# Kernel tuning notes

Hardware: AMD Instinct MI355X
Metric: run time of the kernel (lower is better)

## Reference

```python
import jax, jax.numpy as jnp
import numpy as np

C = 64      # n_feats
DG = 8      # deformable groups
K = 3       # kernel size


def _lrelu(v):
    return jnp.where(v >= 0, v, 0.1 * v)


def _conv3x3(v, w, b):
    out = jax.lax.conv_general_dilated(
        v, w, window_strides=(1, 1), padding=((1, 1), (1, 1)),
        dimension_numbers=('NCHW', 'OIHW', 'NCHW'))
    return out + b[None, :, None, None]


def _up2(v):
    # bilinear upsample x2, align_corners=True (separable gather + lerp)
    B, Cc, H, W = v.shape
    def coords(n):
        c = jnp.arange(2 * n, dtype=jnp.float32) * ((n - 1) / (2 * n - 1))
        i0 = jnp.floor(c).astype(jnp.int32)
        i1 = jnp.minimum(i0 + 1, n - 1)
        f = (c - i0).astype(v.dtype)
        return i0, i1, f
    y0, y1, fy = coords(H)
    x0, x1, fx = coords(W)
    t = v[:, :, y0, :] * (1 - fy)[None, None, :, None] + v[:, :, y1, :] * fy[None, None, :, None]
    return t[:, :, :, x0] * (1 - fx)[None, None, None, :] + t[:, :, :, x1] * fx[None, None, None, :]


def _deform_conv(x, offset, mask, w, b):
    # modulated deformable conv (DCNv2), stride=1, pad=1, dil=1
    B, Cc, H, W = x.shape
    K2 = K * K
    cpg = Cc // DG
    off_y = offset[:, :DG * K2].reshape(B, DG, K2, H, W)
    off_x = offset[:, DG * K2:].reshape(B, DG, K2, H, W)
    m = mask.reshape(B, DG, 1, K2, H, W)
    ky, kx = jnp.meshgrid(jnp.arange(K) - 1, jnp.arange(K) - 1, indexing='ij')
    ky = ky.reshape(K2).astype(x.dtype)
    kx = kx.reshape(K2).astype(x.dtype)
    # absolute sampling positions [B, DG, K2, H, W]
    py = off_y + ky[None, None, :, None, None] + jnp.arange(H, dtype=x.dtype)[None, None, None, :, None]
    px = off_x + kx[None, None, :, None, None] + jnp.arange(W, dtype=x.dtype)[None, None, None, None, :]
    y0f = jnp.floor(py)
    x0f = jnp.floor(px)
    wy = py - y0f
    wx = px - x0f
    y0 = y0f.astype(jnp.int32)
    x0 = x0f.astype(jnp.int32)
    xg = x.reshape(B, DG, cpg, H * W)
    def corner(yi, xi, wgt):
        valid = ((yi >= 0) & (yi < H) & (xi >= 0) & (xi < W)).astype(x.dtype)
        yc = jnp.clip(yi, 0, H - 1)
        xc = jnp.clip(xi, 0, W - 1)
        idx = (yc * W + xc).reshape(B, DG, 1, K2 * H * W)
        g = jnp.take_along_axis(xg, jnp.broadcast_to(idx, (B, DG, cpg, K2 * H * W)), axis=3)
        g = g.reshape(B, DG, cpg, K2, H, W)
        return g * (wgt * valid)[:, :, None]
    val = (corner(y0, x0, (1 - wy) * (1 - wx))
           + corner(y0, x0 + 1, (1 - wy) * wx)
           + corner(y0 + 1, x0, wy * (1 - wx))
           + corner(y0 + 1, x0 + 1, wy * wx))
    val = val * m
    wr = w.reshape(Cc, DG, cpg, K2)
    return jnp.einsum('bgckhw,ogck->bohw', val, wr) + b[None, :, None, None]


def setup_inputs() -> dict:
    key = jax.random.key(0)
    ks = jax.random.split(key, 18)
    B, H, W = 2, 128, 128
    def p(k, shape):
        return jax.random.normal(k, shape, jnp.float32) * 0.05
    return {
        'x': jax.random.normal(ks[0], (B, C, H, W), jnp.float32),
        'y': jax.random.normal(ks[1], (B, C, H, W), jnp.float32),
        'prev_offset': jax.random.normal(ks[2], (B, C, H // 2, W // 2), jnp.float32),
        'prev_stage_fea': jax.random.normal(ks[3], (B, C, H // 2, W // 2), jnp.float32),
        'w1': p(ks[4], (C, 2 * C, 3, 3)), 'b1': jnp.zeros((C,), jnp.float32),
        'w2': p(ks[5], (C, 2 * C, 3, 3)), 'b2': jnp.zeros((C,), jnp.float32),
        'w3': p(ks[6], (C, C, 3, 3)), 'b3': jnp.zeros((C,), jnp.float32),
        'w_off': p(ks[7], (DG * 3 * K * K, C, 3, 3)), 'b_off': jnp.zeros((DG * 3 * K * K,), jnp.float32),
        'w_dcn': p(ks[8], (C, C, 3, 3)), 'b_dcn': jnp.zeros((C,), jnp.float32),
        'w_fea': p(ks[9], (C, 2 * C, 3, 3)), 'b_fea': jnp.zeros((C,), jnp.float32),
    }


def reference(x, y, prev_offset, prev_stage_fea,
              w1, b1, w2, b2, w3, b3, w_off, b_off, w_dcn, b_dcn, w_fea, b_fea):
    prev_offset = _up2(prev_offset)
    off = _lrelu(_conv3x3(jnp.concatenate([x, y], axis=1), w1, b1))
    off = _lrelu(_conv3x3(jnp.concatenate([off, prev_offset * 2], axis=1), w2, b2))
    off = _lrelu(_conv3x3(off, w3, b3))
    # DCNv2Pack: offsets/mask predicted from the offset feature
    co = _conv3x3(off, w_off, b_off)
    o1, o2, m = jnp.split(co, 3, axis=1)
    dcn_offset = jnp.concatenate([o1, o2], axis=1)
    m = jax.nn.sigmoid(m)
    fea = _deform_conv(x, dcn_offset, m, w_dcn, b_dcn)
    prev_fea = _up2(prev_stage_fea)
    out = _lrelu(_conv3x3(jnp.concatenate([fea, prev_fea], axis=1), w_fea, b_fea))
    return (off, out)
```

## Files before the change

### kernel.cpp

```cpp
#include <hip/hip_runtime.h>
#include <math.h>

typedef __bf16 bf16x8 __attribute__((ext_vector_type(8)));
typedef float f32x4 __attribute__((ext_vector_type(4)));
typedef unsigned short u16;
typedef __attribute__((address_space(3))) unsigned int lds_u32;
typedef const __attribute__((address_space(1))) unsigned int glb_u32;

__device__ __forceinline__ u16 f2bf(float f) {
    unsigned int u = __builtin_bit_cast(unsigned int, f);
    unsigned int r = (u + 0x7FFFu + ((u >> 16) & 1u)) >> 16;
    return (u16)r;
}
__device__ __forceinline__ float bf2f(u16 u) {
    unsigned int v = ((unsigned int)u) << 16;
    return __builtin_bit_cast(float, v);
}
__device__ __forceinline__ unsigned int pack2(float a, float b) {
    return (unsigned int)f2bf(a) | ((unsigned int)f2bf(b) << 16);
}
__device__ __forceinline__ bf16x8 ld8(const u16* p) {
    uint4 u = *reinterpret_cast<const uint4*>(p);
    return __builtin_bit_cast(bf16x8, u);
}
__device__ __forceinline__ void gload_lds16(const u16* g, u16* l) {
#if __has_builtin(__builtin_amdgcn_global_load_lds)
    __builtin_amdgcn_global_load_lds((glb_u32*)g, (lds_u32*)l, 16, 0, 0);
#else
    *reinterpret_cast<uint4*>(l) = *reinterpret_cast<const uint4*>(g);
#endif
}

__device__ __forceinline__ void dev_zero(u16* base, int nimg, int C, int B, int tid) {
    int idx = B * 256 + tid;
    int c8 = C >> 3;
    int tot = nimg * 516 * c8;
    if (idx >= tot) return;
    int cb = idx % c8;
    int t = idx / c8;
    int pb = t % 516;
    int img = t / 516;
    int y, x;
    if (pb < 130)      { y = 0;        x = pb; }
    else if (pb < 260) { y = 129;      x = pb - 130; }
    else if (pb < 388) { y = pb - 259; x = 0; }
    else               { y = pb - 387; x = 129; }
    u16* d = base + ((size_t)img * 16900 + (size_t)y * 130 + x) * C + cb * 8;
    uint4 z = {0u, 0u, 0u, 0u};
    *reinterpret_cast<uint4*>(d) = z;
}

__device__ __forceinline__ void dev_repack(const float* w, u16* dst,
                                           int Cout, int Cin, int mode, int B, int tid) {
    int idx = B * 256 + tid;
    int total = Cout * Cin * 9;
    if (idx >= total) return;
    int kk = idx % 9;
    int t = idx / 9;
    int ci = t % Cin;
    int o = t / Cin;
    u16 v = f2bf(w[idx]);
    size_t d;
    if (mode == 0) d = (size_t)o * (9 * Cin) + kk * Cin + ci;
    else           d = (size_t)o * 576 + (ci >> 3) * 72 + kk * 8 + (ci & 7);
    dst[d] = v;
}

__device__ __forceinline__ void dev_to_nhwc8(const float* src, u16* dst,
                                             int c0, int Ctot, int B, int tid) {
    int b = B >> 7;
    int rem = B & 127;
    int q = rem >> 4;
    int p0 = ((rem & 15) * 256 + tid) * 4;
    int y = p0 >> 7, x = p0 & 127;
    const float* s = src + ((size_t)b * 64 + q * 8) * 16384 + p0;
    u16* dbase = dst + (((size_t)b * 16900) + (size_t)(y + 1) * 130 + (x + 1)) * Ctot
                 + c0 + q * 8;
    float4 f[8];
#pragma unroll
    for (int c = 0; c < 8; ++c)
        f[c] = *reinterpret_cast<const float4*>(s + (size_t)c * 16384);
    const float* fp = (const float*)f;
#pragma unroll
    for (int j = 0; j < 4; ++j) {
        uint4 u;
        u.x = pack2(fp[0 * 4 + j], fp[1 * 4 + j]);
        u.y = pack2(fp[2 * 4 + j], fp[3 * 4 + j]);
        u.z = pack2(fp[4 * 4 + j], fp[5 * 4 + j]);
        u.w = pack2(fp[6 * 4 + j], fp[7 * 4 + j]);
        *reinterpret_cast<uint4*>(dbase + (size_t)j * Ctot) = u;
    }
}

__device__ __forceinline__ void dev_up2_8(const float* src, u16* dst,
                                          int c0, int Ctot, float scale, int B, int tid) {
    int b = B >> 9;
    int rem = B & 511;
    int q = rem >> 6;
    int pix = (rem & 63) * 256 + tid;
    int y = pix >> 7, x = pix & 127;
    const float f = 63.0f / 127.0f;
    float cy = y * f, cx = x * f;
    float y0f = floorf(cy), x0f = floorf(cx);
    int y0 = (int)y0f, x0 = (int)x0f;
    int y1 = min(y0 + 1, 63), x1 = min(x0 + 1, 63);
    float fy = cy - y0f, fx = cx - x0f;
    float w00 = (1.f - fy) * (1.f - fx) * scale, w01 = (1.f - fy) * fx * scale;
    float w10 = fy * (1.f - fx) * scale, w11 = fy * fx * scale;
    int i00 = y0 * 64 + x0, i01 = y0 * 64 + x1, i10 = y1 * 64 + x0, i11 = y1 * 64 + x1;
    const float* s = src + ((size_t)b * 64 + q * 8) * 4096;
    float v[8];
#pragma unroll
    for (int c = 0; c < 8; ++c) {
        const float* p = s + (size_t)c * 4096;
        v[c] = w00 * p[i00] + w01 * p[i01] + w10 * p[i10] + w11 * p[i11];
    }
    uint4 u;
    u.x = pack2(v[0], v[1]); u.y = pack2(v[2], v[3]);
    u.z = pack2(v[4], v[5]); u.w = pack2(v[6], v[7]);
    u16* d = dst + (((size_t)b * 16900) + (size_t)(y + 1) * 130 + (x + 1)) * Ctot
             + c0 + q * 8;
    *reinterpret_cast<uint4*>(d) = u;
}

__global__ __launch_bounds__(256) void preproc(
    const float* __restrict__ x, const float* __restrict__ y,
    const float* __restrict__ prev_off, const float* __restrict__ prev_fea,
    const float* __restrict__ w1, const float* __restrict__ w2,
    const float* __restrict__ w3, const float* __restrict__ w_off,
    const float* __restrict__ w_dcn, const float* __restrict__ w_fea,
    u16* __restrict__ T1, u16* __restrict__ T3, u16* __restrict__ T9,
    u16* __restrict__ T4,
    u16* __restrict__ wq1, u16* __restrict__ wq2, u16* __restrict__ wq3,
    u16* __restrict__ wqo, u16* __restrict__ wqd, u16* __restrict__ wqf) {
    int B = blockIdx.x, tid = threadIdx.x;
    if (B < 1024) { dev_up2_8(prev_off, T3, 64, 128, 2.0f, B, tid); return; } B -= 1024;
    if (B < 1024) { dev_up2_8(prev_fea, T9, 64, 128, 1.0f, B, tid); return; } B -= 1024;
    if (B < 256) { dev_to_nhwc8(x, T1, 0, 128, B, tid); return; }       B -= 256;
    if (B < 256) { dev_to_nhwc8(y, T1, 64, 128, B, tid); return; }      B -= 256;
    if (B < 129) { dev_zero(T1, 4, 128, B, tid); return; }  B -= 129;
    if (B < 65)  { dev_zero(T9, 2, 128, B, tid); return; }  B -= 65;
    if (B < 65)  { dev_zero(T4, 4, 64, B, tid); return; }   B -= 65;
    if (B < 288) { dev_repack(w1, wq1, 64, 128, 0, B, tid); return; }   B -= 288;
    if (B < 288) { dev_repack(w2, wq2, 64, 128, 0, B, tid); return; }   B -= 288;
    if (B < 144) { dev_repack(w3, wq3, 64, 64, 0, B, tid); return; }    B -= 144;
    if (B < 486) { dev_repack(w_off, wqo, 216, 64, 0, B, tid); return; } B -= 486;
    if (B < 144) { dev_repack(w_dcn, wqd, 64, 64, 1, B, tid); return; } B -= 144;
    dev_repack(w_fea, wqf, 64, 128, 0, B, tid);
}

template<int CIN, int WAVES, int KSPLIT, int ACTM, bool NHWC_OUT, bool OUT_PAD, int NCHW_MODE>
__global__ __launch_bounds__(WAVES * 64) void conv_tile(
    const u16* __restrict__ in, const u16* __restrict__ wgt,
    const float* __restrict__ bias,
    u16* __restrict__ outN, int c0, int Ctot,
    void* __restrict__ outC, int Cout) {
    constexpr int T = WAVES * 64;
    constexpr int PXW = WAVES / KSPLIT;
    constexpr int BPR = 4 / PXW;
    constexpr int KCH = CIN / KSPLIT;
    constexpr int CSTEPS = KCH / 32;
    constexpr int MSK = (CIN == 128) ? 15 : 7;
    constexpr int RSH = (CIN == 128) ? 8 : 7;
    __shared__ __align__(16) u16 As[2][64 * CIN];

    const int tid = threadIdx.x;
    const int lane = tid & 63;
    const int wv = tid >> 6;
    const int kslice = wv % KSPLIT;
    const int pxc = wv / KSPLIT;
    const int gx = blockIdx.x;
    const int xh = gx % BPR;
    const int y = (gx / BPR) & 127;
    const int b = gx / (BPR * 128);
    const int mblk = blockIdx.y << 6;
    const int n0 = lane & 15;
    const int kq = lane >> 4;
    const int xbase = xh * (PXW * 32) + pxc * 32;

    const u16* inB = in + (size_t)b * 16900 * CIN;

#define STAGE(ss, bf) {                                                        \
        _Pragma("unroll")                                                      \
        for (int i_ = 0; i_ < (8 * CIN) / T; ++i_) {                           \
            int L_ = (i_ * T + tid) * 16;                                      \
            int row_ = L_ >> RSH;                                              \
            int c16_ = (L_ >> 4) & MSK;                                        \
            int sc_ = c16_ ^ (row_ & MSK);                                     \
            const u16* src_ = wgt + (size_t)(mblk + row_) * (9 * CIN)          \
                              + (ss) * CIN + sc_ * 8;                          \
            gload_lds16(src_, &As[bf][L_ >> 1]);                               \
        }                                                                      \
    }

    f32x4 acc[4][2] = {};

    STAGE(0, 0)
    __syncthreads();

    for (int s = 0; s < 9; ++s) {
        const int buf = s & 1;
        if (s < 8) STAGE(s + 1, buf ^ 1)

        const int dy = s / 3, dx = s - dy * 3;
        const u16* brow = inB + ((size_t)(y + dy) * 130 + (xbase + n0 + dx)) * CIN
                          + kq * 8;
        const u16* ab = &As[buf][0];
#pragma unroll
        for (int c = 0; c < CSTEPS; ++c) {
            const int kch = kslice * KCH + c * 32;
            bf16x8 b0 = ld8(brow + kch);
            bf16x8 b1 = ld8(brow + 16 * CIN + kch);
            const int colb = (((kch >> 3) + kq) ^ (n0 & MSK)) * 8;
            bf16x8 a0 = ld8(ab + (0 * 16 + n0) * CIN + colb);
            bf16x8 a1 = ld8(ab + (1 * 16 + n0) * CIN + colb);
            bf16x8 a2 = ld8(ab + (2 * 16 + n0) * CIN + colb);
            bf16x8 a3 = ld8(ab + (3 * 16 + n0) * CIN + colb);
            acc[0][0] = __builtin_amdgcn_mfma_f32_16x16x32_bf16(a0, b0, acc[0][0], 0, 0, 0);
            acc[0][1] = __builtin_amdgcn_mfma_f32_16x16x32_bf16(a0, b1, acc[0][1], 0, 0, 0);
            acc[1][0] = __builtin_amdgcn_mfma_f32_16x16x32_bf16(a1, b0, acc[1][0], 0, 0, 0);
            acc[1][1] = __builtin_amdgcn_mfma_f32_16x16x32_bf16(a1, b1, acc[1][1], 0, 0, 0);
            acc[2][0] = __builtin_amdgcn_mfma_f32_16x16x32_bf16(a2, b0, acc[2][0], 0, 0, 0);
            acc[2][1] = __builtin_amdgcn_mfma_f32_16x16x32_bf16(a2, b1, acc[2][1], 0, 0, 0);
            acc[3][0] = __builtin_amdgcn_mfma_f32_16x16x32_bf16(a3, b0, acc[3][0], 0, 0, 0);
            acc[3][1] = __builtin_amdgcn_mfma_f32_16x16x32_bf16(a3, b1, acc[3][1], 0, 0, 0);
        }
        __syncthreads();
    }
#undef STAGE

    if (KSPLIT == 2) {
        float* red = (float*)(&As[0][0]);
        if (kslice == 1) {
#pragma unroll
            for (int mt = 0; mt < 4; ++mt)
#pragma unroll
                for (int nt = 0; nt < 2; ++nt)
                    *reinterpret_cast<f32x4*>(
                        &red[((pxc * 8) + mt * 2 + nt) * 256 + lane * 4]) = acc[mt][nt];
        }
        __syncthreads();
        if (kslice == 1) return;
#pragma unroll
        for (int mt = 0; mt < 4; ++mt)
#pragma unroll
            for (int nt = 0; nt < 2; ++nt)
                acc[mt][nt] += *reinterpret_cast<const f32x4*>(
                    &red[((pxc * 8) + mt * 2 + nt) * 256 + lane * 4]);
    }

#pragma unroll
    for (int mt = 0; mt < 4; ++mt) {
        const int mbase = mblk + mt * 16 + kq * 4;
        float bs0 = 0.f, bs1 = 0.f, bs2 = 0.f, bs3 = 0.f;
        if (mbase < Cout) {
            bs0 = bias[mbase]; bs1 = bias[mbase + 1];
            bs2 = bias[mbase + 2]; bs3 = bias[mbase + 3];
        }
#pragma unroll
        for (int nt = 0; nt < 2; ++nt) {
            const int xx = xbase + nt * 16 + n0;
            float v0 = acc[mt][nt][0] + bs0, v1 = acc[mt][nt][1] + bs1;
            float v2 = acc[mt][nt][2] + bs2, v3 = acc[mt][nt][3] + bs3;
            if (ACTM == 1) {
                v0 = (v0 >= 0.f) ? v0 : 0.1f * v0;
                v1 = (v1 >= 0.f) ? v1 : 0.1f * v1;
                v2 = (v2 >= 0.f) ? v2 : 0.1f * v2;
                v3 = (v3 >= 0.f) ? v3 : 0.1f * v3;
            } else if (ACTM == 2) {
                if (mbase >= 144) {
                    v0 = 1.f / (1.f + expf(-v0));
                    v1 = 1.f / (1.f + expf(-v1));
                    v2 = 1.f / (1.f + expf(-v2));
                    v3 = 1.f / (1.f + expf(-v3));
                }
            }
            if (NHWC_OUT && mbase < Cout) {
                size_t pix = OUT_PAD ? ((size_t)(y + 1) * 130 + xx + 1)
                                     : ((size_t)y * 128 + xx);
                size_t off = ((size_t)b * (OUT_PAD ? 16900 : 16384) + pix) * Ctot + c0 + mbase;
                uint2 u;
                u.x = pack2(v0, v1); u.y = pack2(v2, v3);
                *reinterpret_cast<uint2*>(outN + off) = u;
            }
            if (NCHW_MODE == 1 && mbase < Cout) {
                float* oc = (float*)outC;
                size_t o = ((size_t)(b * Cout + mbase)) * 16384 + (size_t)y * 128 + xx;
                oc[o] = v0; oc[o + 16384] = v1;
                oc[o + 2 * 16384] = v2; oc[o + 3 * 16384] = v3;
            }
            if (NCHW_MODE == 2 && mbase < Cout) {
                u16* oc = (u16*)outC;
                size_t o = ((size_t)(b * Cout + mbase)) * 16384 + (size_t)y * 128 + xx;
                oc[o] = f2bf(v0); oc[o + 16384] = f2bf(v1);
                oc[o + 2 * 16384] = f2bf(v2); oc[o + 3 * 16384] = f2bf(v3);
            }
        }
    }
}

__global__ __launch_bounds__(256, 2) void dcn_fused(
    const u16* __restrict__ xn, const u16* __restrict__ co,
    const u16* __restrict__ wgt, const float* __restrict__ bias,
    u16* __restrict__ outN) {
    __shared__ u16 lw[64 * 584];
    {
        int t = threadIdx.x;
        int o = t >> 2, chunk = t & 3;
        const u16* src = wgt + o * 576 + chunk * 144;
        u16* dst = lw + o * 584 + chunk * 144;
#pragma unroll
        for (int i = 0; i < 18; ++i)
            *reinterpret_cast<uint4*>(dst + i * 8) =
                *reinterpret_cast<const uint4*>(src + i * 8);
    }
    __syncthreads();

    const int lane = threadIdx.x & 63;
    const int wv = threadIdx.x >> 6;
    const int half = blockIdx.x & 1;
    const int y = (blockIdx.x >> 1) & 127;
    const int b = blockIdx.x >> 8;
    const int n0 = lane & 15;
    const int kq = lane >> 4;
    const int xx = half * 64 + wv * 16 + n0;
    const int p = y * 128 + xx;

    const u16* cob = co + (size_t)b * 216 * 16384 + p;
    const u16* xb = xn + (size_t)b * 16900 * 128;

    float offy[18], offx[18], mvv[18];
#pragma unroll
    for (int cs = 0; cs < 18; ++cs) {
        int gk8 = cs * 4 + kq;
        offy[cs] = bf2f(cob[(size_t)gk8 * 16384]);
        offx[cs] = bf2f(cob[(size_t)(72 + gk8) * 16384]);
        mvv[cs]  = bf2f(cob[(size_t)(144 + gk8) * 16384]);
    }

    f32x4 acc[4] = {};
    float w00[2], w01[2], w10[2], w11[2];
    uint4 q00[2], q01[2], q10[2], q11[2];

#define DCN_GL(cs, st) {                                                       \
        int gk8_ = (cs) * 4 + kq;                                              \
        int g_ = (gk8_ * 57) >> 9;                                             \
        int kk_ = gk8_ - 9 * g_;                                               \
        int ky_ = (kk_ * 11) >> 5;                                             \
        int kx_ = kk_ - 3 * ky_;                                               \
        float py_ = offy[cs] + (float)(ky_ - 1) + (float)y;                    \
        float px_ = offx[cs] + (float)(kx_ - 1) + (float)xx;                   \
        float y0f_ = floorf(py_), x0f_ = floorf(px_);                          \
        float wy_ = py_ - y0f_, wx_ = px_ - x0f_;                              \
        int y0_ = (int)y0f_, x0_ = (int)x0f_, y1_ = y0_ + 1, x1_ = x0_ + 1;    \
        float m00_ = ((unsigned)y0_ < 128u && (unsigned)x0_ < 128u) ? 1.f : 0.f; \
        float m01_ = ((unsigned)y0_ < 128u && (unsigned)x1_ < 128u) ? 1.f : 0.f; \
        float m10_ = ((unsigned)y1_ < 128u && (unsigned)x0_ < 128u) ? 1.f : 0.f; \
        float m11_ = ((unsigned)y1_ < 128u && (unsigned)x1_ < 128u) ? 1.f : 0.f; \
        float mv_ = mvv[cs];                                                   \
        w00[st] = (1.f - wy_) * (1.f - wx_) * m00_ * mv_;                      \
        w01[st] = (1.f - wy_) * wx_ * m01_ * mv_;                              \
        w10[st] = wy_ * (1.f - wx_) * m10_ * mv_;                              \
        w11[st] = wy_ * wx_ * m11_ * mv_;                                      \
        int y0c_ = min(max(y0_, 0), 127), y1c_ = min(max(y1_, 0), 127);        \
        int x0c_ = min(max(x0_, 0), 127), x1c_ = min(max(x1_, 0), 127);        \
        const u16* xg_ = xb + g_ * 8;                                          \
        q00[st] = *reinterpret_cast<const uint4*>(xg_ + ((size_t)(y0c_ + 1) * 130 + x0c_ + 1) * 128); \
        q01[st] = *reinterpret_cast<const uint4*>(xg_ + ((size_t)(y0c_ + 1) * 130 + x1c_ + 1) * 128); \
        q10[st] = *reinterpret_cast<const uint4*>(xg_ + ((size_t)(y1c_ + 1) * 130 + x0c_ + 1) * 128); \
        q11[st] = *reinterpret_cast<const uint4*>(xg_ + ((size_t)(y1c_ + 1) * 130 + x1c_ + 1) * 128); \
    }

#define DCN_GU(cs, st) {                                                       \
        const unsigned int* a00_ = &q00[st].x; const unsigned int* a01_ = &q01[st].x; \
        const unsigned int* a10_ = &q10[st].x; const unsigned int* a11_ = &q11[st].x; \
        float r_[8];                                                           \
        _Pragma("unroll")                                                      \
        for (int c = 0; c < 8; ++c) {                                          \
            unsigned int u00_ = a00_[c >> 1], u01_ = a01_[c >> 1];             \
            unsigned int u10_ = a10_[c >> 1], u11_ = a11_[c >> 1];             \
            int sh_ = (c & 1) * 16;                                            \
            float f00_ = bf2f((u16)(u00_ >> sh_)), f01_ = bf2f((u16)(u01_ >> sh_)); \
            float f10_ = bf2f((u16)(u10_ >> sh_)), f11_ = bf2f((u16)(u11_ >> sh_)); \
            r_[c] = w00[st] * f00_ + w01[st] * f01_ + w10[st] * f10_ + w11[st] * f11_; \
        }                                                                      \
        uint4 bu_;                                                             \
        bu_.x = pack2(r_[0], r_[1]); bu_.y = pack2(r_[2], r_[3]);              \
        bu_.z = pack2(r_[4], r_[5]); bu_.w = pack2(r_[6], r_[7]);              \
        bf16x8 bfrag_ = __builtin_bit_cast(bf16x8, bu_);                       \
        const int kcol_ = (cs) * 32 + kq * 8;                                  \
        bf16x8 a0_ = ld8(lw + (size_t)(0 * 16 + n0) * 584 + kcol_);            \
        bf16x8 a1_ = ld8(lw + (size_t)(1 * 16 + n0) * 584 + kcol_);            \
        bf16x8 a2_ = ld8(lw + (size_t)(2 * 16 + n0) * 584 + kcol_);            \
        bf16x8 a3_ = ld8(lw + (size_t)(3 * 16 + n0) * 584 + kcol_);            \
        acc[0] = __builtin_amdgcn_mfma_f32_16x16x32_bf16(a0_, bfrag_, acc[0], 0, 0, 0); \
        acc[1] = __builtin_amdgcn_mfma_f32_16x16x32_bf16(a1_, bfrag_, acc[1], 0, 0, 0); \
        acc[2] = __builtin_amdgcn_mfma_f32_16x16x32_bf16(a2_, bfrag_, acc[2], 0, 0, 0); \
        acc[3] = __builtin_amdgcn_mfma_f32_16x16x32_bf16(a3_, bfrag_, acc[3], 0, 0, 0); \
    }

    DCN_GL(0, 0)
    DCN_GL(1, 1)
#pragma unroll
    for (int cs = 0; cs < 18; cs += 2) {
        DCN_GU(cs, 0)
        if (cs + 2 < 18) DCN_GL(cs + 2, 0)
        DCN_GU(cs + 1, 1)
        if (cs + 3 < 18) DCN_GL(cs + 3, 1)
    }
#undef DCN_GL
#undef DCN_GU

#pragma unroll
    for (int mt = 0; mt < 4; ++mt) {
        const int mbase = mt * 16 + kq * 4;
        float v0 = acc[mt][0] + bias[mbase];
        float v1 = acc[mt][1] + bias[mbase + 1];
        float v2 = acc[mt][2] + bias[mbase + 2];
        float v3 = acc[mt][3] + bias[mbase + 3];
        size_t off = ((size_t)b * 16900 + (size_t)(y + 1) * 130 + (xx + 1)) * 128 + mbase;
        uint2 u;
        u.x = pack2(v0, v1); u.y = pack2(v2, v3);
        *reinterpret_cast<uint2*>(outN + off) = u;
    }
}

#define T1_OFF 0u
#define T3_OFF 8652800u
#define T9_OFF 17305600u
#define T4_OFF 25958400u
#define T5_OFF 30284800u
#define T6_OFF 34611200u
#define W1_OFF 48766976u
#define W2_OFF 48914432u
#define W3_OFF 49061888u
#define WF_OFF 49135616u
#define WO_OFF 49283072u
#define WD_OFF 49577984u

extern "C" void kernel_launch(void* const* d_in, const int* in_sizes, int n_in,
                              void* d_out, int out_size, void* d_ws, size_t ws_size,
                              hipStream_t stream) {
    const float* x        = (const float*)d_in[0];
    const float* y        = (const float*)d_in[1];
    const float* prev_off = (const float*)d_in[2];
    const float* prev_fea = (const float*)d_in[3];
    const float* w1 = (const float*)d_in[4];  const float* b1 = (const float*)d_in[5];
    const float* w2 = (const float*)d_in[6];  const float* b2 = (const float*)d_in[7];
    const float* w3 = (const float*)d_in[8];  const float* b3 = (const float*)d_in[9];
    const float* w_off = (const float*)d_in[10]; const float* b_off = (const float*)d_in[11];
    const float* w_dcn = (const float*)d_in[12]; const float* b_dcn = (const float*)d_in[13];
    const float* w_fea = (const float*)d_in[14]; const float* b_fea = (const float*)d_in[15];

    float* out_off = (float*)d_out;
    float* out_out = (float*)d_out + (size_t)2 * 64 * 16384;

    char* ws = (char*)d_ws;
    u16* T1 = (u16*)(ws + T1_OFF);
    u16* T3 = (u16*)(ws + T3_OFF);
    u16* T9 = (u16*)(ws + T9_OFF);
    u16* T4 = (u16*)(ws + T4_OFF);
    u16* T5 = (u16*)(ws + T5_OFF);
    u16* T6 = (u16*)(ws + T6_OFF);
    u16* wq1 = (u16*)(ws + W1_OFF);
    u16* wq2 = (u16*)(ws + W2_OFF);
    u16* wq3 = (u16*)(ws + W3_OFF);
    u16* wqf = (u16*)(ws + WF_OFF);
    u16* wqo = (u16*)(ws + WO_OFF);
    u16* wqd = (u16*)(ws + WD_OFF);

    preproc<<<dim3(4457), dim3(256), 0, stream>>>(
        x, y, prev_off, prev_fea, w1, w2, w3, w_off, w_dcn, w_fea,
        T1, T3, T9, T4, wq1, wq2, wq3, wqo, wqd, wqf);

    conv_tile<128, 8, 2, 1, true, true, 0><<<dim3(256, 1), dim3(512), 0, stream>>>(
        T1, wq1, b1, T3, 0, 128, nullptr, 64);
    conv_tile<128, 8, 2, 1, true, true, 0><<<dim3(256, 1), dim3(512), 0, stream>>>(
        T3, wq2, b2, T4, 0, 64, nullptr, 64);
    conv_tile<64, 4, 1, 1, true, true, 1><<<dim3(256, 1), dim3(256), 0, stream>>>(
        T4, wq3, b3, T5, 0, 64, out_off, 64);
    conv_tile<64, 4, 1, 2, false, false, 2><<<dim3(256, 4), dim3(256), 0, stream>>>(
        T5, wqo, b_off, nullptr, 0, 0, T6, 216);
    dcn_fused<<<dim3(512), dim3(256), 0, stream>>>(T1, T6, wqd, b_dcn, T9);
    conv_tile<128, 8, 2, 1, false, false, 1><<<dim3(256, 1), dim3(512), 0, stream>>>(
        T9, wqf, b_fea, nullptr, 0, 0, out_out, 64);
}
```

Baseline: 132.0 us.

## Fuse offset/mask conv into deformable conv kernel via shared-memory handoff

Merges the 216-channel offset/mask convolution into the DCN kernel. Each block first computes the offsets and sigmoid masks for its 64 pixels into LDS, then runs the deformable sampling and MFMA directly from LDS, so the T6 intermediate no longer makes a round trip through global memory and one launch is removed. DCN weights are now read from global or cache instead of being staged in LDS, which frees LDS for the offset tile. The risks are the extra LDS footprint (about 60KB), which may limit occupancy, and the first phase having four waves cover 256 output channels, of which only 216 are used.

```diff
diff --git a/kernel.cpp b/kernel.cpp
--- a/kernel.cpp
+++ b/kernel.cpp
@@ -267,13 +267,6 @@
                 v1 = (v1 >= 0.f) ? v1 : 0.1f * v1;
                 v2 = (v2 >= 0.f) ? v2 : 0.1f * v2;
                 v3 = (v3 >= 0.f) ? v3 : 0.1f * v3;
-            } else if (ACTM == 2) {
-                if (mbase >= 144) {
-                    v0 = 1.f / (1.f + expf(-v0));
-                    v1 = 1.f / (1.f + expf(-v1));
-                    v2 = 1.f / (1.f + expf(-v2));
-                    v3 = 1.f / (1.f + expf(-v3));
-                }
             }
             if (NHWC_OUT && mbase < Cout) {
                 size_t pix = OUT_PAD ? ((size_t)(y + 1) * 130 + xx + 1)
@@ -289,53 +282,124 @@
                 oc[o] = v0; oc[o + 16384] = v1;
                 oc[o + 2 * 16384] = v2; oc[o + 3 * 16384] = v3;
             }
-            if (NCHW_MODE == 2 && mbase < Cout) {
-                u16* oc = (u16*)outC;
-                size_t o = ((size_t)(b * Cout + mbase)) * 16384 + (size_t)y * 128 + xx;
-                oc[o] = f2bf(v0); oc[o + 16384] = f2bf(v1);
-                oc[o + 2 * 16384] = f2bf(v2); oc[o + 3 * 16384] = f2bf(v3);
-            }
-        }
-    }
-}
-
-__global__ __launch_bounds__(256, 2) void dcn_fused(
-    const u16* __restrict__ xn, const u16* __restrict__ co,
-    const u16* __restrict__ wgt, const float* __restrict__ bias,
+        }
+    }
+}
+
+#define COST 220
+__global__ __launch_bounds__(256, 2) void cofu(
+    const u16* __restrict__ off5,
+    const u16* __restrict__ wgo,
+    const float* __restrict__ bo,
+    const u16* __restrict__ xn,
+    const u16* __restrict__ wgd,
+    const float* __restrict__ bd,
     u16* __restrict__ outN) {
-    __shared__ u16 lw[64 * 584];
-    {
-        int t = threadIdx.x;
-        int o = t >> 2, chunk = t & 3;
-        const u16* src = wgt + o * 576 + chunk * 144;
-        u16* dst = lw + o * 584 + chunk * 144;
-#pragma unroll
-        for (int i = 0; i < 18; ++i)
-            *reinterpret_cast<uint4*>(dst + i * 8) =
-                *reinterpret_cast<const uint4*>(src + i * 8);
-    }
-    __syncthreads();
-
-    const int lane = threadIdx.x & 63;
-    const int wv = threadIdx.x >> 6;
+    __shared__ __align__(16) u16 coL[64 * COST];
+    __shared__ __align__(16) u16 As[16384];
+
+    const int tid = threadIdx.x;
+    const int lane = tid & 63;
+    const int wv = tid >> 6;
     const int half = blockIdx.x & 1;
     const int y = (blockIdx.x >> 1) & 127;
     const int b = blockIdx.x >> 8;
     const int n0 = lane & 15;
     const int kq = lane >> 4;
+
+    {
+        const u16* inB = off5 + (size_t)b * 16900 * 64;
+        f32x4 acc[4][2][2] = {};
+
+#define OSTAGE(ss) {                                                           \
+            _Pragma("unroll")                                                  \
+            for (int i_ = 0; i_ < 8; ++i_) {                                   \
+                int L_ = (i_ * 256 + tid) * 16;                                \
+                int row_ = L_ >> 7;                                            \
+                int c16_ = (L_ >> 4) & 7;                                      \
+                int sc_ = c16_ ^ (row_ & 7);                                   \
+                const u16* src_ = wgo + (size_t)row_ * 576 + (ss) * 64 + sc_ * 8; \
+                gload_lds16(src_, &As[L_ >> 1]);                               \
+            }                                                                  \
+        }
+
+        OSTAGE(0)
+        __syncthreads();
+        for (int s = 0; s < 9; ++s) {
+            const int dy = s / 3, dx = s - dy * 3;
+            const u16* ab = &As[(size_t)wv * 64 * 64];
+#pragma unroll
+            for (int c2 = 0; c2 < 2; ++c2) {
+                const int xx0 = half * 64 + c2 * 32 + n0 + dx;
+                const u16* brow = inB + ((size_t)(y + dy) * 130 + xx0) * 64 + kq * 8;
+#pragma unroll
+                for (int c = 0; c < 2; ++c) {
+                    const int kch = c * 32;
+                    bf16x8 b0 = ld8(brow + kch);
+                    bf16x8 b1 = ld8(brow + 16 * 64 + kch);
+                    const int colb = (((kch >> 3) + kq) ^ (n0 & 7)) * 8;
+                    bf16x8 a0 = ld8(ab + (0 * 16 + n0) * 64 + colb);
+                    bf16x8 a1 = ld8(ab + (1 * 16 + n0) * 64 + colb);
+                    bf16x8 a2 = ld8(ab + (2 * 16 + n0) * 64 + colb);
+                    bf16x8 a3 = ld8(ab + (3 * 16 + n0) * 64 + colb);
+                    acc[0][c2][0] = __builtin_amdgcn_mfma_f32_16x16x32_bf16(a0, b0, acc[0][c2][0], 0, 0, 0);
+                    acc[0][c2][1] = __builtin_amdgcn_mfma_f32_16x16x32_bf16(a0, b1, acc[0][c2][1], 0, 0, 0);
+                    acc[1][c2][0] = __builtin_amdgcn_mfma_f32_16x16x32_bf16(a1, b0, acc[1][c2][0], 0, 0, 0);
+                    acc[1][c2][1] = __builtin_amdgcn_mfma_f32_16x16x32_bf16(a1, b1, acc[1][c2][1], 0, 0, 0);
+                    acc[2][c2][0] = __builtin_amdgcn_mfma_f32_16x16x32_bf16(a2, b0, acc[2][c2][0], 0, 0, 0);
+                    acc[2][c2][1] = __builtin_amdgcn_mfma_f32_16x16x32_bf16(a2, b1, acc[2][c2][1], 0, 0, 0);
+                    acc[3][c2][0] = __builtin_amdgcn_mfma_f32_16x16x32_bf16(a3, b0, acc[3][c2][0], 0, 0, 0);
+                    acc[3][c2][1] = __builtin_amdgcn_mfma_f32_16x16x32_bf16(a3, b1, acc[3][c2][1], 0, 0, 0);
+                }
+            }
+            if (s < 8) {
+                __syncthreads();
+                OSTAGE(s + 1)
+                __syncthreads();
+            }
+        }
+#undef OSTAGE
+
+#pragma unroll
+        for (int mt = 0; mt < 4; ++mt) {
+            const int ch = wv * 64 + mt * 16 + kq * 4;
+            if (ch < 216) {
+                float bs0 = bo[ch], bs1 = bo[ch + 1], bs2 = bo[ch + 2], bs3 = bo[ch + 3];
+#pragma unroll
+                for (int c2 = 0; c2 < 2; ++c2)
+#pragma unroll
+                    for (int nt = 0; nt < 2; ++nt) {
+                        const int pl = c2 * 32 + nt * 16 + n0;
+                        float v0 = acc[mt][c2][nt][0] + bs0;
+                        float v1 = acc[mt][c2][nt][1] + bs1;
+                        float v2 = acc[mt][c2][nt][2] + bs2;
+                        float v3 = acc[mt][c2][nt][3] + bs3;
+                        if (ch >= 144) {
+                            v0 = 1.f / (1.f + expf(-v0));
+                            v1 = 1.f / (1.f + expf(-v1));
+                            v2 = 1.f / (1.f + expf(-v2));
+                            v3 = 1.f / (1.f + expf(-v3));
+                        }
+                        uint2 u;
+                        u.x = pack2(v0, v1); u.y = pack2(v2, v3);
+                        *reinterpret_cast<uint2*>(&coL[(size_t)pl * COST + ch]) = u;
+                    }
+            }
+        }
+        __syncthreads();
+    }
+
     const int xx = half * 64 + wv * 16 + n0;
-    const int p = y * 128 + xx;
-
-    const u16* cob = co + (size_t)b * 216 * 16384 + p;
+    const int pl = wv * 16 + n0;
     const u16* xb = xn + (size_t)b * 16900 * 128;
 
     float offy[18], offx[18], mvv[18];
 #pragma unroll
     for (int cs = 0; cs < 18; ++cs) {
         int gk8 = cs * 4 + kq;
-        offy[cs] = bf2f(cob[(size_t)gk8 * 16384]);
-        offx[cs] = bf2f(cob[(size_t)(72 + gk8) * 16384]);
-        mvv[cs]  = bf2f(cob[(size_t)(144 + gk8) * 16384]);
+        offy[cs] = bf2f(coL[(size_t)pl * COST + gk8]);
+        offx[cs] = bf2f(coL[(size_t)pl * COST + 72 + gk8]);
+        mvv[cs]  = bf2f(coL[(size_t)pl * COST + 144 + gk8]);
     }
 
     f32x4 acc[4] = {};
@@ -389,10 +453,10 @@
         bu_.z = pack2(r_[4], r_[5]); bu_.w = pack2(r_[6], r_[7]);              \
         bf16x8 bfrag_ = __builtin_bit_cast(bf16x8, bu_);                       \
         const int kcol_ = (cs) * 32 + kq * 8;                                  \
-        bf16x8 a0_ = ld8(lw + (size_t)(0 * 16 + n0) * 584 + kcol_);            \
-        bf16x8 a1_ = ld8(lw + (size_t)(1 * 16 + n0) * 584 + kcol_);            \
-        bf16x8 a2_ = ld8(lw + (size_t)(2 * 16 + n0) * 584 + kcol_);            \
-        bf16x8 a3_ = ld8(lw + (size_t)(3 * 16 + n0) * 584 + kcol_);            \
+        bf16x8 a0_ = ld8(wgd + (size_t)(0 * 16 + n0) * 576 + kcol_);           \
+        bf16x8 a1_ = ld8(wgd + (size_t)(1 * 16 + n0) * 576 + kcol_);           \
+        bf16x8 a2_ = ld8(wgd + (size_t)(2 * 16 + n0) * 576 + kcol_);           \
+        bf16x8 a3_ = ld8(wgd + (size_t)(3 * 16 + n0) * 576 + kcol_);           \
         acc[0] = __builtin_amdgcn_mfma_f32_16x16x32_bf16(a0_, bfrag_, acc[0], 0, 0, 0); \
         acc[1] = __builtin_amdgcn_mfma_f32_16x16x32_bf16(a1_, bfrag_, acc[1], 0, 0, 0); \
         acc[2] = __builtin_amdgcn_mfma_f32_16x16x32_bf16(a2_, bfrag_, acc[2], 0, 0, 0); \
@@ -414,10 +478,10 @@
 #pragma unroll
     for (int mt = 0; mt < 4; ++mt) {
         const int mbase = mt * 16 + kq * 4;
-        float v0 = acc[mt][0] + bias[mbase];
-        float v1 = acc[mt][1] + bias[mbase + 1];
-        float v2 = acc[mt][2] + bias[mbase + 2];
-        float v3 = acc[mt][3] + bias[mbase + 3];
+        float v0 = acc[mt][0] + bd[mbase];
+        float v1 = acc[mt][1] + bd[mbase + 1];
+        float v2 = acc[mt][2] + bd[mbase + 2];
+        float v3 = acc[mt][3] + bd[mbase + 3];
         size_t off = ((size_t)b * 16900 + (size_t)(y + 1) * 130 + (xx + 1)) * 128 + mbase;
         uint2 u;
         u.x = pack2(v0, v1); u.y = pack2(v2, v3);
@@ -430,13 +494,12 @@
 #define T9_OFF 17305600u
 #define T4_OFF 25958400u
 #define T5_OFF 30284800u
-#define T6_OFF 34611200u
-#define W1_OFF 48766976u
-#define W2_OFF 48914432u
-#define W3_OFF 49061888u
-#define WF_OFF 49135616u
-#define WO_OFF 49283072u
-#define WD_OFF 49577984u
+#define W1_OFF 34611200u
+#define W2_OFF 34758656u
+#define W3_OFF 34906112u
+#define WF_OFF 34979840u
+#define WO_OFF 35127296u
+#define WD_OFF 35422208u
 
 extern "C" void kernel_launch(void* const* d_in, const int* in_sizes, int n_in,
                               void* d_out, int out_size, void* d_ws, size_t ws_size,
@@ -461,7 +524,6 @@
     u16* T9 = (u16*)(ws + T9_OFF);
     u16* T4 = (u16*)(ws + T4_OFF);
     u16* T5 = (u16*)(ws + T5_OFF);
-    u16* T6 = (u16*)(ws + T6_OFF);
     u16* wq1 = (u16*)(ws + W1_OFF);
     u16* wq2 = (u16*)(ws + W2_OFF);
     u16* wq3 = (u16*)(ws + W3_OFF);
@@ -479,9 +541,8 @@
         T3, wq2, b2, T4, 0, 64, nullptr, 64);
     conv_tile<64, 4, 1, 1, true, true, 1><<<dim3(256, 1), dim3(256), 0, stream>>>(
         T4, wq3, b3, T5, 0, 64, out_off, 64);
-    conv_tile<64, 4, 1, 2, false, false, 2><<<dim3(256, 4), dim3(256), 0, stream>>>(
-        T5, wqo, b_off, nullptr, 0, 0, T6, 216);
-    dcn_fused<<<dim3(512), dim3(256), 0, stream>>>(T1, T6, wqd, b_dcn, T9);
+    cofu<<<dim3(512), dim3(256), 0, stream>>>(
+        T5, wqo, b_off, T1, wqd, b_dcn, T9);
     conv_tile<128, 8, 2, 1, false, false, 1><<<dim3(256, 1), dim3(512), 0, stream>>>(
         T9, wqf, b_fea, nullptr, 0, 0, out_out, 64);
 }
```

Measured after the change: 140.6 us. +6.5%, slower.
